# Optimization experiments

Hardware: AMD Instinct MI355X
Metric: run time of the kernel (lower is better)

Reference implementation:

```python
import jax, jax.numpy as jnp
import numpy as np

B, T, D = 8, 2048, 1024


def setup_inputs() -> dict:
    key = jax.random.key(0)
    ks = jax.random.split(key, 9)
    s = 1.0 / np.sqrt(D)
    return {
        "e": jax.random.normal(ks[0], (B, T, D), jnp.float32),
        "residual": jax.random.normal(ks[1], (B, T, D), jnp.float32),
        "Wq_w": jax.random.normal(ks[2], (D, D), jnp.float32) * s,
        "Wq_b": jax.random.normal(ks[3], (D,), jnp.float32) * s,
        "Wk_w": jax.random.normal(ks[4], (D, D), jnp.float32) * s,
        "Wk_b": jax.random.normal(ks[5], (D,), jnp.float32) * s,
        "Wv_w": jax.random.normal(ks[6], (D, D), jnp.float32) * s,
        "Wv_b": jax.random.normal(ks[7], (D,), jnp.float32) * s,
        "v_table": jax.random.normal(ks[8], (T, 1), jnp.float32),
    }


def reference(e, residual, Wq_w, Wq_b, Wk_w, Wk_b, Wv_w, Wv_b, v_table):
    T_ = e.shape[1]
    # relative position index: pos[i,j] = max(i - j, 0)
    pos = jnp.arange(T_)
    rel = jnp.maximum(pos[:, None] - pos[None, :], 0)          # (T, T) int
    pos_embd = v_table[rel, 0]                                 # (T, T) gather from Embedding(length, 1)

    # torch Linear: x @ W.T + b
    Q = e @ Wq_w.T + Wq_b                                      # (B, T, D)
    K = residual @ Wk_w.T + Wk_b                               # (B, T, D)
    V = e @ Wv_w.T + Wv_b                                      # (B, T, D)

    # Q @ K^T  (torch: Q @ Wk(residual).transpose(-2,-1))
    scores = jnp.einsum('btd,bsd->bts', Q, K)                  # (B, T, T)
    # einsum('BeT,Tt->BTt', K^T, pos_embd) == sum_e K[B,T,e] * pos_embd[T,t]
    scores = scores + K.sum(-1)[:, :, None] * pos_embd[None]   # (B, T, T)

    # causal mask via tril (zeros strictly-upper entries); NO softmax in this variant
    scores = scores * jnp.tril(jnp.ones((T_, T_), scores.dtype))
    return scores @ V                                          # (B, T, D)
```

## Files before the change

kernel.cpp:

```cpp
#include <hip/hip_runtime.h>

typedef unsigned short u16;
typedef __attribute__((ext_vector_type(8))) short bf16x8;
typedef __attribute__((ext_vector_type(8))) unsigned short u16x8;
typedef __attribute__((ext_vector_type(4))) float f32x4;

static __device__ __forceinline__ u16 f2bf(float f) {
  unsigned u = __float_as_uint(f);
  u += 0x7FFFu + ((u >> 16) & 1u);
  return (u16)(u >> 16);
}
static __device__ __forceinline__ float bf2f(u16 h) {
  return __uint_as_float(((unsigned)h) << 16);
}

__global__ __launch_bounds__(256) void conv_big(const float* __restrict__ e,
                                                const float* __restrict__ res,
                                                u16* __restrict__ eb, u16* __restrict__ rb) {
  int i = blockIdx.x * 256 + threadIdx.x;
  const float* in = blockIdx.z ? res : e;
  u16* out = blockIdx.z ? rb : eb;
  const float4* p = (const float4*)in + (size_t)i * 2;
  float4 a = p[0], b = p[1];
  u16x8 r;
  r[0] = f2bf(a.x); r[1] = f2bf(a.y); r[2] = f2bf(a.z); r[3] = f2bf(a.w);
  r[4] = f2bf(b.x); r[5] = f2bf(b.y); r[6] = f2bf(b.z); r[7] = f2bf(b.w);
  ((u16x8*)out)[i] = r;
}
__global__ __launch_bounds__(256) void conv_w(const float* __restrict__ w0,
                                              const float* __restrict__ w1,
                                              const float* __restrict__ w2,
                                              u16* __restrict__ o0, u16* __restrict__ o1,
                                              u16* __restrict__ o2) {
  int i = blockIdx.x * 256 + threadIdx.x;
  const float* in = blockIdx.z == 0 ? w0 : (blockIdx.z == 1 ? w1 : w2);
  u16* out = blockIdx.z == 0 ? o0 : (blockIdx.z == 1 ? o1 : o2);
  const float4* p = (const float4*)in + (size_t)i * 2;
  float4 a = p[0], b = p[1];
  u16x8 r;
  r[0] = f2bf(a.x); r[1] = f2bf(a.y); r[2] = f2bf(a.z); r[3] = f2bf(a.w);
  r[4] = f2bf(b.x); r[5] = f2bf(b.y); r[6] = f2bf(b.z); r[7] = f2bf(b.w);
  ((u16x8*)out)[i] = r;
}

__global__ __launch_bounds__(256) void ksum_kernel(const u16* __restrict__ K,
                                                   float* __restrict__ out) {
  int row = blockIdx.x * 4 + (threadIdx.x >> 6);
  int lane = threadIdx.x & 63;
  const u16x8* p = (const u16x8*)(K + (size_t)row * 1024);
  float s = 0.f;
#pragma unroll
  for (int it = 0; it < 2; ++it) {
    u16x8 v = p[lane + it * 64];
#pragma unroll
    for (int j = 0; j < 8; ++j) s += bf2f(v[j]);
  }
#pragma unroll
  for (int off = 32; off >= 1; off >>= 1) s += __shfl_down(s, off);
  if (lane == 0) out[row] = s;
}

enum { M_BIASN = 0, M_BIASM = 1, M_SCORES = 2, M_OUT = 3 };

template <int MODE>
static __device__ __forceinline__ void core128(
    const u16* __restrict__ Ab, int lda, const u16* __restrict__ Bb, int ldb,
    char* smem, int m0, int n0, int nk, void* __restrict__ Cbase, int ldc,
    const float* __restrict__ bias, const float* __restrict__ ksb,
    const float* __restrict__ vtab) {
  const int tid = threadIdx.x;
  const int lane = tid & 63;
  const int wid = tid >> 6;
  const int wm = wid >> 1, wn = wid & 1;

  char* As = smem;
  char* Bs = smem + 16384;

  const int rbase_st = tid >> 3;
  const int gcol = ((tid & 7) << 4) ^ ((rbase_st & 7) << 4);

  const int aoff = (wm * 64 + (lane & 15)) * 128;
  const int boff = (wn * 64 + (lane & 15)) * 128;
  const int c0 = ((0 * 4 + (lane >> 4)) ^ (lane & 7)) << 4;
  const int c1 = ((1 * 4 + (lane >> 4)) ^ (lane & 7)) << 4;

  f32x4 acc[4][4];
#pragma unroll
  for (int m = 0; m < 4; ++m)
#pragma unroll
    for (int n = 0; n < 4; ++n) acc[m][n] = (f32x4){0.f, 0.f, 0.f, 0.f};

  for (int kt = 0; kt < nk; ++kt) {
    const int k0 = kt * 64;
#pragma unroll
    for (int i = 0; i < 4; ++i) {
      const char* ga = (const char*)(Ab + (size_t)(m0 + i * 32 + rbase_st) * lda + k0) + gcol;
      __builtin_amdgcn_global_load_lds(
          (const __attribute__((address_space(1))) void*)ga,
          (__attribute__((address_space(3))) void*)(As + i * 4096 + wid * 1024), 16, 0, 0);
    }
#pragma unroll
    for (int i = 0; i < 4; ++i) {
      const char* gb = (const char*)(Bb + (size_t)(n0 + i * 32 + rbase_st) * ldb + k0) + gcol;
      __builtin_amdgcn_global_load_lds(
          (const __attribute__((address_space(1))) void*)gb,
          (__attribute__((address_space(3))) void*)(Bs + i * 4096 + wid * 1024), 16, 0, 0);
    }
    __syncthreads();
#pragma unroll
    for (int ks = 0; ks < 2; ++ks) {
      const int cks = ks ? c1 : c0;
      bf16x8 af[4], bfv[4];
#pragma unroll
      for (int m = 0; m < 4; ++m) af[m] = *(const bf16x8*)(As + aoff + m * 2048 + cks);
#pragma unroll
      for (int n = 0; n < 4; ++n) bfv[n] = *(const bf16x8*)(Bs + boff + n * 2048 + cks);
#pragma unroll
      for (int m = 0; m < 4; ++m)
#pragma unroll
        for (int n = 0; n < 4; ++n)
          acc[m][n] = __builtin_amdgcn_mfma_f32_16x16x32_bf16(af[m], bfv[n], acc[m][n], 0, 0, 0);
    }
    __syncthreads();
  }

  u16* C16 = (u16*)Cbase;
  float* Cf = (float*)Cbase;
#pragma unroll
  for (int m = 0; m < 4; ++m) {
#pragma unroll
    for (int n = 0; n < 4; ++n) {
      const int rb = m0 + wm * 64 + m * 16 + ((lane >> 4) << 2);
      const int c = n0 + wn * 64 + n * 16 + (lane & 15);
#pragma unroll
      for (int j = 0; j < 4; ++j) {
        const int r = rb + j;
        float v = acc[m][n][j];
        if (MODE == M_BIASN) {
          v += bias[c];
          C16[(size_t)r * ldc + c] = f2bf(v);
        } else if (MODE == M_BIASM) {
          v += bias[r];
          C16[(size_t)r * ldc + c] = f2bf(v);
        } else if (MODE == M_SCORES) {
          if (c <= r) v += ksb[r] * vtab[r - c];
          else v = 0.f;
          C16[(size_t)r * ldc + c] = f2bf(v);
        } else {
          Cf[(size_t)r * ldc + c] = v;
        }
      }
    }
  }
}

static __device__ __forceinline__ int2 xcd_swz_xy() {
  const int nl = gridDim.x * gridDim.y;
  const int l = blockIdx.x + gridDim.x * blockIdx.y;
  const int logical = (l & 7) * (nl >> 3) + (l >> 3);
  return make_int2(logical % gridDim.x, logical / gridDim.x);
}

__global__ __launch_bounds__(256, 3) void k_qk_proj(
    const u16* eb, const u16* rb, const u16* Wq, const u16* Wk,
    const float* bq, const float* bk, u16* Q, u16* K) {
  int2 g = xcd_swz_xy();
  const int zz = blockIdx.z;
  const u16* A = zz ? rb : eb;
  const u16* B = zz ? Wk : Wq;
  const float* bias = zz ? bk : bq;
  u16* C = zz ? K : Q;
  __shared__ char smem[32768];
  core128<M_BIASN>(A, 1024, B, 1024, smem, g.y * 128, g.x * 128, 16,
                   C, 1024, bias, nullptr, nullptr);
}
__global__ __launch_bounds__(256, 3) void k_v_proj(
    const u16* Wv, const u16* eb, u16* VT, const float* bv) {
  int2 g = xcd_swz_xy();
  __shared__ char smem[32768];
  core128<M_BIASM>(Wv, 1024, eb, 1024, smem, g.y * 128, g.x * 128, 16,
                   VT, 16384, bv, nullptr, nullptr);
}
__global__ __launch_bounds__(256, 3) void k_scores(
    const u16* Q, const u16* K, u16* S, const float* ksum, const float* vtab) {
  const int h = (blockIdx.x & 7) * 17 + (blockIdx.x >> 3);
  int gy = 0;
#pragma unroll
  for (int q = 1; q < 16; ++q) if (q * (q + 1) / 2 <= h) gy = q;
  const int gx = h - gy * (gy + 1) / 2;
  const int z = blockIdx.z;
  __shared__ char smem[32768];
  core128<M_SCORES>(Q + (size_t)z * 2048 * 1024, 1024,
                    K + (size_t)z * 2048 * 1024, 1024, smem,
                    gy * 128, gx * 128, 16,
                    S + (size_t)z * 2048 * 2048, 2048,
                    nullptr, ksum + (size_t)z * 2048, vtab);
}
__global__ __launch_bounds__(256, 3) void k_out(
    const u16* S, const u16* VT, float* O) {
  int2 g = xcd_swz_xy();
  const int gx = g.x;
  const int p = g.y;
  const int z = blockIdx.z;
  __shared__ char smem[32768];
#pragma unroll
  for (int sub = 0; sub < 2; ++sub) {
    const int gy = sub ? 15 - p : p;
    const int nk = (gy + 1) * 2;
    core128<M_OUT>(S + (size_t)z * 2048 * 2048, 2048,
                   VT + (size_t)z * 2048, 16384, smem,
                   gy * 128, gx * 128, nk,
                   O + (size_t)z * 2048 * 1024, 1024,
                   nullptr, nullptr, nullptr);
    if (sub == 0) __syncthreads();
  }
}

extern "C" void kernel_launch(void* const* d_in, const int* in_sizes, int n_in,
                              void* d_out, int out_size, void* d_ws, size_t ws_size,
                              hipStream_t stream) {
  (void)in_sizes; (void)n_in; (void)out_size; (void)ws_size;
  const float* e    = (const float*)d_in[0];
  const float* res  = (const float*)d_in[1];
  const float* Wq_w = (const float*)d_in[2];
  const float* Wq_b = (const float*)d_in[3];
  const float* Wk_w = (const float*)d_in[4];
  const float* Wk_b = (const float*)d_in[5];
  const float* Wv_w = (const float*)d_in[6];
  const float* Wv_b = (const float*)d_in[7];
  const float* vtab = (const float*)d_in[8];

  char* ws = (char*)d_ws;
  const size_t SZ = 33554432;
  u16* ebf = (u16*)(ws);
  u16* rbf = (u16*)(ws + SZ);
  u16* Qb  = (u16*)(ws + 2 * SZ);
  u16* Kb  = (u16*)(ws + 3 * SZ);
  u16* VT  = (u16*)(ws + 4 * SZ);
  u16* Wqb = (u16*)(ws + 5 * SZ);
  u16* Wkb = (u16*)(ws + 5 * SZ + 2097152);
  u16* Wvb = (u16*)(ws + 5 * SZ + 2 * 2097152);
  float* ksum = (float*)(ws + 5 * SZ + 3 * 2097152);
  u16* scores = (u16*)(ws);

  conv_big<<<dim3(8192, 1, 2), 256, 0, stream>>>(e, res, ebf, rbf);
  conv_w<<<dim3(512, 1, 3), 256, 0, stream>>>(Wq_w, Wk_w, Wv_w, Wqb, Wkb, Wvb);

  k_qk_proj<<<dim3(8, 128, 2), 256, 0, stream>>>(ebf, rbf, Wqb, Wkb, Wq_b, Wk_b, Qb, Kb);
  k_v_proj<<<dim3(128, 8, 1), 256, 0, stream>>>(Wvb, ebf, VT, Wv_b);

  ksum_kernel<<<4096, 256, 0, stream>>>(Kb, ksum);

  k_scores<<<dim3(136, 1, 8), 256, 0, stream>>>(Qb, Kb, scores, ksum, vtab);

  k_out<<<dim3(8, 8, 8), 256, 0, stream>>>(scores, VT, (float*)d_out);
}
```

Before: 292.4 us.

## Flatten grids with XCD-aware block mapping and split paired output tiles

```diff
diff --git a/kernel.cpp b/kernel.cpp
--- a/kernel.cpp
+++ b/kernel.cpp
@@ -154,41 +154,44 @@
   }
 }
 
-static __device__ __forceinline__ int2 xcd_swz_xy() {
-  const int nl = gridDim.x * gridDim.y;
-  const int l = blockIdx.x + gridDim.x * blockIdx.y;
-  const int logical = (l & 7) * (nl >> 3) + (l >> 3);
-  return make_int2(logical % gridDim.x, logical / gridDim.x);
-}
-
-__global__ __launch_bounds__(256, 3) void k_qk_proj(
+__global__ __launch_bounds__(256, 4) void k_qk_proj(
     const u16* eb, const u16* rb, const u16* Wq, const u16* Wk,
     const float* bq, const float* bk, u16* Q, u16* K) {
-  int2 g = xcd_swz_xy();
-  const int zz = blockIdx.z;
-  const u16* A = zz ? rb : eb;
-  const u16* B = zz ? Wk : Wq;
-  const float* bias = zz ? bk : bq;
-  u16* C = zz ? K : Q;
-  __shared__ char smem[32768];
-  core128<M_BIASN>(A, 1024, B, 1024, smem, g.y * 128, g.x * 128, 16,
+  const int l = blockIdx.x;
+  const int xcd = l & 7;
+  const int idx = l >> 3;
+  const bool isK = idx >= 128;
+  const int j = idx & 127;
+  const int gy = xcd * 16 + (j >> 3);
+  const int gx = j & 7;
+  const u16* A = isK ? rb : eb;
+  const u16* B = isK ? Wk : Wq;
+  const float* bias = isK ? bk : bq;
+  u16* C = isK ? K : Q;
+  __shared__ char smem[32768];
+  core128<M_BIASN>(A, 1024, B, 1024, smem, gy * 128, gx * 128, 16,
                    C, 1024, bias, nullptr, nullptr);
 }
-__global__ __launch_bounds__(256, 3) void k_v_proj(
+__global__ __launch_bounds__(256, 4) void k_v_proj(
     const u16* Wv, const u16* eb, u16* VT, const float* bv) {
-  int2 g = xcd_swz_xy();
-  __shared__ char smem[32768];
-  core128<M_BIASM>(Wv, 1024, eb, 1024, smem, g.y * 128, g.x * 128, 16,
+  const int l = blockIdx.x;
+  const int xcd = l & 7;
+  const int idx = l >> 3;
+  const int gxt = xcd * 16 + (idx >> 3);
+  const int gyd = idx & 7;
+  __shared__ char smem[32768];
+  core128<M_BIASM>(Wv, 1024, eb, 1024, smem, gyd * 128, gxt * 128, 16,
                    VT, 16384, bv, nullptr, nullptr);
 }
-__global__ __launch_bounds__(256, 3) void k_scores(
+__global__ __launch_bounds__(256, 4) void k_scores(
     const u16* Q, const u16* K, u16* S, const float* ksum, const float* vtab) {
-  const int h = (blockIdx.x & 7) * 17 + (blockIdx.x >> 3);
+  const int l = blockIdx.x;
+  const int z = l & 7;
+  const int h = l >> 3;
   int gy = 0;
 #pragma unroll
   for (int q = 1; q < 16; ++q) if (q * (q + 1) / 2 <= h) gy = q;
   const int gx = h - gy * (gy + 1) / 2;
-  const int z = blockIdx.z;
   __shared__ char smem[32768];
   core128<M_SCORES>(Q + (size_t)z * 2048 * 1024, 1024,
                     K + (size_t)z * 2048 * 1024, 1024, smem,
@@ -196,24 +199,20 @@
                     S + (size_t)z * 2048 * 2048, 2048,
                     nullptr, ksum + (size_t)z * 2048, vtab);
 }
-__global__ __launch_bounds__(256, 3) void k_out(
+__global__ __launch_bounds__(256, 4) void k_out(
     const u16* S, const u16* VT, float* O) {
-  int2 g = xcd_swz_xy();
-  const int gx = g.x;
-  const int p = g.y;
-  const int z = blockIdx.z;
-  __shared__ char smem[32768];
-#pragma unroll
-  for (int sub = 0; sub < 2; ++sub) {
-    const int gy = sub ? 15 - p : p;
-    const int nk = (gy + 1) * 2;
-    core128<M_OUT>(S + (size_t)z * 2048 * 2048, 2048,
-                   VT + (size_t)z * 2048, 16384, smem,
-                   gy * 128, gx * 128, nk,
-                   O + (size_t)z * 2048 * 1024, 1024,
-                   nullptr, nullptr, nullptr);
-    if (sub == 0) __syncthreads();
-  }
+  const int l = blockIdx.x;
+  const int z = l & 7;
+  const int idx = l >> 3;
+  const int gy = 15 - (idx >> 3);
+  const int gx = idx & 7;
+  const int nk = (gy + 1) * 2;
+  __shared__ char smem[32768];
+  core128<M_OUT>(S + (size_t)z * 2048 * 2048, 2048,
+                 VT + (size_t)z * 2048, 16384, smem,
+                 gy * 128, gx * 128, nk,
+                 O + (size_t)z * 2048 * 1024, 1024,
+                 nullptr, nullptr, nullptr);
 }
 
 extern "C" void kernel_launch(void* const* d_in, const int* in_sizes, int n_in,
@@ -246,12 +245,12 @@
   conv_big<<<dim3(8192, 1, 2), 256, 0, stream>>>(e, res, ebf, rbf);
   conv_w<<<dim3(512, 1, 3), 256, 0, stream>>>(Wq_w, Wk_w, Wv_w, Wqb, Wkb, Wvb);
 
-  k_qk_proj<<<dim3(8, 128, 2), 256, 0, stream>>>(ebf, rbf, Wqb, Wkb, Wq_b, Wk_b, Qb, Kb);
-  k_v_proj<<<dim3(128, 8, 1), 256, 0, stream>>>(Wvb, ebf, VT, Wv_b);
+  k_qk_proj<<<dim3(2048, 1, 1), 256, 0, stream>>>(ebf, rbf, Wqb, Wkb, Wq_b, Wk_b, Qb, Kb);
+  k_v_proj<<<dim3(1024, 1, 1), 256, 0, stream>>>(Wvb, ebf, VT, Wv_b);
 
   ksum_kernel<<<4096, 256, 0, stream>>>(Kb, ksum);
 
-  k_scores<<<dim3(136, 1, 8), 256, 0, stream>>>(Qb, Kb, scores, ksum, vtab);
-
-  k_out<<<dim3(8, 8, 8), 256, 0, stream>>>(scores, VT, (float*)d_out);
-}
+  k_scores<<<dim3(1088, 1, 1), 256, 0, stream>>>(Qb, Kb, scores, ksum, vtab);
+
+  k_out<<<dim3(1024, 1, 1), 256, 0, stream>>>(scores, VT, (float*)d_out);
+}
```

New measurement: 256.6 us. 12.2% less time.
